# Kernel optimization log

Measured on AMD Instinct MI355X. Metric: run time of the kernel, lower is better.

## Reference

```python
import jax, jax.numpy as jnp
import numpy as np

SHIFT = 1e-09  # input_shift


def _patches(v, kh, kw):
    # v: (B, C, H, W) -> (B, C, kh*kw, Ho, Wo), VALID padding, stride 1
    B, C, H, W = v.shape
    Ho, Wo = H - kh + 1, W - kw + 1
    cols = [v[:, :, i:i + Ho, j:j + Wo] for i in range(kh) for j in range(kw)]
    return jnp.stack(cols, axis=2)


def setup_inputs() -> dict:
    key = jax.random.key(0)
    kx, k1k, k2k, kb = jax.random.split(key, 4)
    B, C, H, W = 32, 64, 64, 64
    kh, kw, F = 3, 3, 128
    x = jax.random.normal(kx, (B, C, H, W), dtype=jnp.float32)
    # log-domain kernels (learned params of the two Add modules)
    k1 = jax.random.normal(k1k, (kh, kw, C, F), dtype=jnp.float32) * 0.1
    k2 = jax.random.normal(k2k, (kh, kw, C, F), dtype=jnp.float32) * 0.1
    bias = jnp.zeros((F,), dtype=jnp.float32)
    return {"x": x, "k1": k1, "k2": k2, "bias": bias}


def reference(x, k1, k2, bias):
    kh, kw, C, F = k1.shape
    # Ln: log of ReLU'd patches (positive and negative parts of x)
    ep_pos = jnp.exp(jnp.log(jax.nn.relu(_patches(x, kh, kw)) + SHIFT))   # (B,C,kh*kw,Ho,Wo)
    ep_neg = jnp.exp(jnp.log(jax.nn.relu(_patches(-x, kh, kw)) + SHIFT))
    # Add + Exp + patch reduction: sum_p exp(ln_patch + k) == einsum(exp(ln_patch), exp(k))
    ek1 = jnp.exp(k1).reshape(kh * kw, C, F)
    ek2 = jnp.exp(k2).reshape(kh * kw, C, F)
    y11 = jnp.einsum('bckhw,kcf->bfhw', ep_pos, ek1)
    y12 = jnp.einsum('bckhw,kcf->bfhw', ep_pos, ek2)
    y21 = jnp.einsum('bckhw,kcf->bfhw', ep_neg, ek1)
    y22 = jnp.einsum('bckhw,kcf->bfhw', ep_neg, ek2)
    return y11 - y12 - y21 + y22 + bias[None, :, None, None]
```

## Files before the change

kernel.cpp:

```cpp
#include <hip/hip_runtime.h>
#include <hip/hip_bf16.h>

typedef __attribute__((ext_vector_type(4))) float f32x4;
typedef __attribute__((ext_vector_type(8))) short bf16x8;

static __device__ __forceinline__ unsigned int f2bf(float f) {
    unsigned int u = __float_as_uint(f);
    return (u + 0x7FFFu + ((u >> 16) & 1u)) >> 16;
}

static __device__ __forceinline__ void gload_lds16(const void* g, void* l) {
    __builtin_amdgcn_global_load_lds(
        (const __attribute__((address_space(1))) unsigned int*)g,
        (__attribute__((address_space(3))) unsigned int*)l, 16, 0, 0);
}

__global__ __launch_bounds__(256) void wprep_kernel(const float* __restrict__ k1,
                                                    const float* __restrict__ k2,
                                                    unsigned short* __restrict__ wq) {
    int g = blockIdx.x * 256 + threadIdx.x;
    if (g >= 9216) return;
    int cc = g & 7;
    int f  = (g >> 3) & 127;
    int p  = g >> 10;
    unsigned int w[4];
#pragma unroll
    for (int e2 = 0; e2 < 4; ++e2) {
        int s0 = (p * 64 + cc * 8 + e2 * 2) * 128 + f;
        unsigned int lo = f2bf(expf(k1[s0]) - expf(k2[s0]));
        int s1 = s0 + 128;
        unsigned int hh = f2bf(expf(k1[s1]) - expf(k2[s1]));
        w[e2] = lo | (hh << 16);
    }
    *(uint4*)(wq + p * 8192 + f * 64 + ((cc * 8) ^ ((f & 7) << 3))) =
        *(const uint4*)w;
}

__global__ __launch_bounds__(256) void xprep_kernel(const float* __restrict__ x,
                                                    unsigned short* __restrict__ xsw) {
    __shared__ float t[64][65];
    int b = blockIdx.x >> 6;
    int h = blockIdx.x & 63;
    const float* xb = x + b * 262144 + h * 64;
    int tid = threadIdx.x;
    int col4 = (tid & 15) * 4;
    int c0   = tid >> 4;
#pragma unroll
    for (int i = 0; i < 4; ++i) {
        int c = c0 + i * 16;
        f32x4 v = *(const f32x4*)(xb + c * 4096 + col4);
        t[c][col4 + 0] = v[0]; t[c][col4 + 1] = v[1];
        t[c][col4 + 2] = v[2]; t[c][col4 + 3] = v[3];
    }
    __syncthreads();
    unsigned short* orow = xsw + ((size_t)(b * 64 + h)) * 4096;
#pragma unroll
    for (int i = 0; i < 2; ++i) {
        int j   = tid + i * 256;
        int col = j >> 3;
        int cb  = ((j & 7) ^ (col & 7)) * 8;
        uint4 pk;
        pk.x = f2bf(t[cb + 0][col]) | (f2bf(t[cb + 1][col]) << 16);
        pk.y = f2bf(t[cb + 2][col]) | (f2bf(t[cb + 3][col]) << 16);
        pk.z = f2bf(t[cb + 4][col]) | (f2bf(t[cb + 5][col]) << 16);
        pk.w = f2bf(t[cb + 6][col]) | (f2bf(t[cb + 7][col]) << 16);
        *(uint4*)(orow + j * 8) = pk;
    }
}

__global__ __launch_bounds__(256, 2) void conv_kernel(const unsigned short* __restrict__ xsw,
                                                      const unsigned short* __restrict__ wq,
                                                      const float* __restrict__ bias,
                                                      float* __restrict__ out) {
    __shared__ unsigned short xs[6 * 64 * 64];
    __shared__ unsigned short bs[2][128 * 64];

    int bid0 = blockIdx.x;
    int bid  = (bid0 & 7) * 64 + (bid0 >> 3);
    int b    = bid >> 4;
    int tile = bid & 15;
    int oh0  = tile * 4;

    int tid  = threadIdx.x;
    int lane = tid & 63;
    int wid  = tid >> 6;
    int wr   = wid >> 1;
    int wc   = wid & 1;
    int lr   = lane & 15;
    int hi   = lane >> 4;

    {
        const unsigned short* srcb = xsw + (size_t)b * 262144;
#pragma unroll
        for (int i = 0; i < 12; ++i) {
            int chunk = i * 4 + wid;
            int row   = chunk >> 3;
            int srow  = oh0 + row; if (srow > 63) srow = 63;
            gload_lds16((const char*)(srcb + srow * 4096) + (chunk & 7) * 1024 + lane * 16,
                        (char*)xs + chunk * 1024);
        }
#pragma unroll
        for (int i = 0; i < 4; ++i) {
            int chunk = i * 4 + wid;
            gload_lds16((const char*)wq + chunk * 1024 + lane * 16,
                        (char*)bs[0] + chunk * 1024);
        }
    }

    f32x4 acc[4][8];
#pragma unroll
    for (int ni = 0; ni < 4; ++ni)
#pragma unroll
        for (int q = 0; q < 8; ++q) acc[ni][q] = (f32x4){0.f, 0.f, 0.f, 0.f};

#pragma unroll
    for (int p = 0; p < 9; ++p) {
        asm volatile("s_waitcnt vmcnt(0)" ::: "memory");
        __builtin_amdgcn_s_barrier();
        __builtin_amdgcn_sched_barrier(0);
        if (p < 8) {
#pragma unroll
            for (int i = 0; i < 4; ++i) {
                int chunk = i * 4 + wid;
                gload_lds16((const char*)wq + (p + 1) * 16384 + chunk * 1024 + lane * 16,
                            (char*)bs[(p + 1) & 1] + chunk * 1024);
            }
        }
        const int ki = p / 3, kj = p % 3;
        const unsigned short* bc = bs[p & 1];
#pragma unroll
        for (int kb = 0; kb < 2; ++kb) {
            int c0 = kb * 32 + hi * 8;
            bf16x8 bfr[4];
#pragma unroll
            for (int ni = 0; ni < 4; ++ni) {
                int f = wc * 64 + ni * 16 + lr;
                bfr[ni] = *(const bf16x8*)(&bc[f * 64 + (c0 ^ ((f & 7) << 3))]);
            }
#pragma unroll
            for (int oh2 = 0; oh2 < 2; ++oh2) {
                int row = wr * 2 + oh2 + ki;
#pragma unroll
                for (int mi = 0; mi < 4; ++mi) {
                    int col  = mi * 16 + lr + kj;
                    int colc = col > 63 ? 63 : col;
                    bf16x8 af = *(const bf16x8*)(&xs[((row * 64 + colc) << 6) + (c0 ^ ((colc & 7) << 3))]);
#pragma unroll
                    for (int ni = 0; ni < 4; ++ni)
                        acc[ni][oh2 * 4 + mi] = __builtin_amdgcn_mfma_f32_16x16x32_bf16(
                            bfr[ni], af, acc[ni][oh2 * 4 + mi], 0, 0, 0);
                }
            }
        }
    }

    float* ob = out + b * 492032;
#pragma unroll
    for (int ni = 0; ni < 4; ++ni) {
        int fb = wc * 64 + ni * 16 + (hi << 2);
        f32x4 bv4 = *(const f32x4*)(bias + fb);
#pragma unroll
        for (int t = 0; t < 4; ++t) {
#pragma unroll
            for (int oh2 = 0; oh2 < 2; ++oh2) {
                int oh = oh0 + wr * 2 + oh2;
                if (oh < 62) {
                    float* orow = ob + ((fb + t) * 62 + oh) * 62;
#pragma unroll
                    for (int mi = 0; mi < 4; ++mi) {
                        int ow = mi * 16 + lr;
                        if (ow < 62) orow[ow] = acc[ni][oh2 * 4 + mi][t] + bv4[t];
                    }
                }
            }
        }
    }
}

extern "C" void kernel_launch(void* const* d_in, const int* in_sizes, int n_in,
                              void* d_out, int out_size, void* d_ws, size_t ws_size,
                              hipStream_t stream) {
    const float* x    = (const float*)d_in[0];
    const float* k1   = (const float*)d_in[1];
    const float* k2   = (const float*)d_in[2];
    const float* bias = (const float*)d_in[3];
    float* out = (float*)d_out;

    unsigned short* wq  = (unsigned short*)d_ws;
    unsigned short* xsw = (unsigned short*)d_ws + 73728;

    hipLaunchKernelGGL(wprep_kernel, dim3(36), dim3(256), 0, stream, k1, k2, wq);
    hipLaunchKernelGGL(xprep_kernel, dim3(2048), dim3(256), 0, stream, x, xsw);
    hipLaunchKernelGGL(conv_kernel, dim3(512), dim3(256), 0, stream, xsw, wq, bias, out);
}
```

Baseline: 118.3 us.

## Load weight fragments straight to registers and merge prep kernels

The conv kernel no longer stages the per-tap weight tile through a double-buffered LDS area. Each lane now loads its own B fragments from global memory into a register double buffer using inline global_load_dwordx4, which removes the per-tap LDS reads and the block barriers inside the tap loop. The weight-prep and x-prep kernels are merged into one launch, and the weight layout becomes unswizzled and split by k-block to match the register loads. In exchange, every wave re-reads the weights from L2, register pressure rises with 16 extra fragment registers, and vmcnt(0) waits still serialize each tap on the prefetch.

After: 114.8 us. 3.0% less time.

```diff
diff --git a/kernel.cpp b/kernel.cpp
--- a/kernel.cpp
+++ b/kernel.cpp
@@ -15,34 +15,36 @@
         (__attribute__((address_space(3))) unsigned int*)l, 16, 0, 0);
 }
 
-__global__ __launch_bounds__(256) void wprep_kernel(const float* __restrict__ k1,
-                                                    const float* __restrict__ k2,
-                                                    unsigned short* __restrict__ wq) {
-    int g = blockIdx.x * 256 + threadIdx.x;
-    if (g >= 9216) return;
-    int cc = g & 7;
-    int f  = (g >> 3) & 127;
-    int p  = g >> 10;
-    unsigned int w[4];
+__global__ __launch_bounds__(256) void prep_kernel(const float* __restrict__ x,
+                                                   const float* __restrict__ k1,
+                                                   const float* __restrict__ k2,
+                                                   unsigned short* __restrict__ xsw,
+                                                   unsigned short* __restrict__ wq) {
+    __shared__ float t[64][65];
+    int blk = blockIdx.x;
+    int tid = threadIdx.x;
+    if (blk >= 2048) {
+        int g = (blk - 2048) * 256 + tid;
+        if (g >= 9216) return;
+        int ch8 = g & 3;
+        int f   = (g >> 2) & 127;
+        int kb  = (g >> 9) & 1;
+        int p   = g >> 10;
+        unsigned int w[4];
 #pragma unroll
-    for (int e2 = 0; e2 < 4; ++e2) {
-        int s0 = (p * 64 + cc * 8 + e2 * 2) * 128 + f;
-        unsigned int lo = f2bf(expf(k1[s0]) - expf(k2[s0]));
-        int s1 = s0 + 128;
-        unsigned int hh = f2bf(expf(k1[s1]) - expf(k2[s1]));
-        w[e2] = lo | (hh << 16);
+        for (int e2 = 0; e2 < 4; ++e2) {
+            int c  = kb * 32 + ch8 * 8 + e2 * 2;
+            int s0 = (p * 64 + c) * 128 + f;
+            unsigned int lo = f2bf(expf(k1[s0]) - expf(k2[s0]));
+            unsigned int hh = f2bf(expf(k1[s0 + 128]) - expf(k2[s0 + 128]));
+            w[e2] = lo | (hh << 16);
+        }
+        *(uint4*)(wq + ((p * 2 + kb) * 128 + f) * 32 + ch8 * 8) = *(const uint4*)w;
+        return;
     }
-    *(uint4*)(wq + p * 8192 + f * 64 + ((cc * 8) ^ ((f & 7) << 3))) =
-        *(const uint4*)w;
-}
-
-__global__ __launch_bounds__(256) void xprep_kernel(const float* __restrict__ x,
-                                                    unsigned short* __restrict__ xsw) {
-    __shared__ float t[64][65];
-    int b = blockIdx.x >> 6;
-    int h = blockIdx.x & 63;
+    int b = blk >> 6;
+    int h = blk & 63;
     const float* xb = x + b * 262144 + h * 64;
-    int tid = threadIdx.x;
     int col4 = (tid & 15) * 4;
     int c0   = tid >> 4;
 #pragma unroll
@@ -73,7 +75,6 @@
                                                       const float* __restrict__ bias,
                                                       float* __restrict__ out) {
     __shared__ unsigned short xs[6 * 64 * 64];
-    __shared__ unsigned short bs[2][128 * 64];
 
     int bid0 = blockIdx.x;
     int bid  = (bid0 & 7) * 64 + (bid0 >> 3);
@@ -99,13 +100,17 @@
             gload_lds16((const char*)(srcb + srow * 4096) + (chunk & 7) * 1024 + lane * 16,
                         (char*)xs + chunk * 1024);
         }
+    }
+
+    const unsigned short* wl = wq + (wc * 64 + lr) * 32 + hi * 8;
+    bf16x8 wfrag[2][8];
 #pragma unroll
-        for (int i = 0; i < 4; ++i) {
-            int chunk = i * 4 + wid;
-            gload_lds16((const char*)wq + chunk * 1024 + lane * 16,
-                        (char*)bs[0] + chunk * 1024);
-        }
-    }
+    for (int kb = 0; kb < 2; ++kb)
+#pragma unroll
+        for (int ni = 0; ni < 4; ++ni)
+            asm volatile("global_load_dwordx4 %0, %1, off"
+                         : "=&v"(wfrag[0][kb * 4 + ni])
+                         : "v"(wl + kb * 4096 + ni * 512) : "memory");
 
     f32x4 acc[4][8];
 #pragma unroll
@@ -113,30 +118,30 @@
 #pragma unroll
         for (int q = 0; q < 8; ++q) acc[ni][q] = (f32x4){0.f, 0.f, 0.f, 0.f};
 
+    asm volatile("s_waitcnt vmcnt(0)" ::: "memory");
+    __builtin_amdgcn_s_barrier();
+    __builtin_amdgcn_sched_barrier(0);
+
 #pragma unroll
     for (int p = 0; p < 9; ++p) {
-        asm volatile("s_waitcnt vmcnt(0)" ::: "memory");
-        __builtin_amdgcn_s_barrier();
-        __builtin_amdgcn_sched_barrier(0);
+        const int cur = p & 1, nxt = cur ^ 1;
+        if (p > 0) {
+            asm volatile("s_waitcnt vmcnt(0)" ::: "memory");
+            __builtin_amdgcn_sched_barrier(0);
+        }
         if (p < 8) {
 #pragma unroll
-            for (int i = 0; i < 4; ++i) {
-                int chunk = i * 4 + wid;
-                gload_lds16((const char*)wq + (p + 1) * 16384 + chunk * 1024 + lane * 16,
-                            (char*)bs[(p + 1) & 1] + chunk * 1024);
-            }
+            for (int kb = 0; kb < 2; ++kb)
+#pragma unroll
+                for (int ni = 0; ni < 4; ++ni)
+                    asm volatile("global_load_dwordx4 %0, %1, off"
+                                 : "=&v"(wfrag[nxt][kb * 4 + ni])
+                                 : "v"(wl + (p + 1) * 8192 + kb * 4096 + ni * 512) : "memory");
         }
         const int ki = p / 3, kj = p % 3;
-        const unsigned short* bc = bs[p & 1];
 #pragma unroll
         for (int kb = 0; kb < 2; ++kb) {
             int c0 = kb * 32 + hi * 8;
-            bf16x8 bfr[4];
-#pragma unroll
-            for (int ni = 0; ni < 4; ++ni) {
-                int f = wc * 64 + ni * 16 + lr;
-                bfr[ni] = *(const bf16x8*)(&bc[f * 64 + (c0 ^ ((f & 7) << 3))]);
-            }
 #pragma unroll
             for (int oh2 = 0; oh2 < 2; ++oh2) {
                 int row = wr * 2 + oh2 + ki;
@@ -148,7 +153,7 @@
 #pragma unroll
                     for (int ni = 0; ni < 4; ++ni)
                         acc[ni][oh2 * 4 + mi] = __builtin_amdgcn_mfma_f32_16x16x32_bf16(
-                            bfr[ni], af, acc[ni][oh2 * 4 + mi], 0, 0, 0);
+                            wfrag[cur][kb * 4 + ni], af, acc[ni][oh2 * 4 + mi], 0, 0, 0);
                 }
             }
         }
@@ -189,7 +194,6 @@
     unsigned short* wq  = (unsigned short*)d_ws;
     unsigned short* xsw = (unsigned short*)d_ws + 73728;
 
-    hipLaunchKernelGGL(wprep_kernel, dim3(36), dim3(256), 0, stream, k1, k2, wq);
-    hipLaunchKernelGGL(xprep_kernel, dim3(2048), dim3(256), 0, stream, x, xsw);
+    hipLaunchKernelGGL(prep_kernel, dim3(2084), dim3(256), 0, stream, x, k1, k2, xsw, wq);
     hipLaunchKernelGGL(conv_kernel, dim3(512), dim3(256), 0, stream, xsw, wq, bias, out);
 }
```
